# Kernel tuning notes

Hardware: AMD Instinct MI355X
Metric: run time of the kernel (lower is better)

Reference implementation:

```python
import jax, jax.numpy as jnp
import numpy as np

NUM_EMBEDDINGS = 1024
EMBEDDING_DIM = 64
COMMITMENT_COST = 0.25


def setup_inputs() -> dict:
    key = jax.random.key(0)
    k1, k2 = jax.random.split(key)
    inputs = jax.random.normal(k1, (16, 64, 64, 64), dtype=jnp.float32)
    codebook = jax.random.normal(k2, (EMBEDDING_DIM, NUM_EMBEDDINGS), dtype=jnp.float32) * 0.01
    return {"inputs": inputs, "codebook": codebook}


def reference(inputs, codebook):
    # flatten exactly as torch: reshape(-1, D) on (B,C,H,W)
    flat = inputs.reshape(-1, EMBEDDING_DIM)  # [N, D]
    distances = (jnp.sum(flat * flat, axis=1, keepdims=True)
                 + jnp.sum(codebook * codebook, axis=0, keepdims=True)
                 - 2.0 * jnp.matmul(flat, codebook))
    encoding_indices = jnp.argmin(distances, axis=1)  # [N]
    quantized = codebook[:, encoding_indices].T.reshape(inputs.shape)
    # losses (MSE over all elements)
    codebook_loss = jnp.mean((jax.lax.stop_gradient(quantized) - inputs) ** 2)
    commitment_loss = COMMITMENT_COST * jnp.mean((quantized - jax.lax.stop_gradient(inputs)) ** 2)
    # perplexity from codebook usage histogram
    n = encoding_indices.shape[0]
    counts = jnp.zeros((NUM_EMBEDDINGS,), dtype=jnp.float32).at[encoding_indices].add(1.0)
    avg_probs = counts / n
    entropy = -jnp.sum(avg_probs * jnp.log(avg_probs + 1e-10))
    perplexity = jnp.exp(entropy)
    # straight-through estimator
    ste = inputs + jax.lax.stop_gradient(quantized - inputs)
    return (ste, perplexity, codebook_loss, commitment_loss,
            encoding_indices.reshape(inputs.shape[0], -1))
```

## Files before the change

kernel.cpp:

```cpp
#include <hip/hip_runtime.h>

typedef __attribute__((ext_vector_type(8))) short short8;
typedef __attribute__((ext_vector_type(4))) float f32x4;

#define N_ROWS   65536
#define DIM      64
#define K_CODES  1024
#define TOTAL_ELEMS 4194304
#define THETA    1e-3f


__device__ __forceinline__ unsigned short f2bf(float f) {
    union { float f; unsigned int u; } c; c.f = f;
    unsigned int u = c.u;
    return (unsigned short)((u + 0x7fffu + ((u >> 16) & 1u)) >> 16);
}
__device__ __forceinline__ float bf2f(unsigned short b) {
    union { unsigned int u; float f; } c; c.u = ((unsigned int)b) << 16;
    return c.f;
}
__device__ __forceinline__ f32x4 MFMA(short8 a, short8 b, f32x4 c) {
    return __builtin_amdgcn_mfma_f32_16x16x32_bf16(a, b, c, 0, 0, 0);
}

__global__ __launch_bounds__(128) void k_prep(const float* __restrict__ cb,
                                              float* __restrict__ norms,
                                              int* __restrict__ counts,
                                              float* __restrict__ cbT,
                                              unsigned short* __restrict__ cb_hi,
                                              unsigned short* __restrict__ cb_lo,
                                              int* __restrict__ flagcnt) {
    int k = blockIdx.x * 128 + threadIdx.x;
    float v0 = cb[k];
    float s = __fmul_rn(v0, v0);
    cbT[k * DIM] = v0;
    {
        float t = -2.0f * v0;
        unsigned short hb = f2bf(t);
        cb_hi[k * DIM] = hb;
        cb_lo[k * DIM] = f2bf(t - bf2f(hb));
    }
#pragma unroll 4
    for (int d = 1; d < DIM; ++d) {
        float v = cb[d * K_CODES + k];
        s = __fadd_rn(s, __fmul_rn(v, v));
        cbT[k * DIM + d] = v;
        float t = -2.0f * v;
        unsigned short hb = f2bf(t);
        cb_hi[k * DIM + d] = hb;
        cb_lo[k * DIM + d] = f2bf(t - bf2f(hb));
    }
    norms[k] = s;
    counts[k] = 0;
    if (k == 0) flagcnt[0] = 0;
}

__global__ __launch_bounds__(256, 2) void k_assign(const float* __restrict__ x,
                                                   const float* __restrict__ norms,
                                                   const unsigned short* __restrict__ cb_hi,
                                                   const unsigned short* __restrict__ cb_lo,
                                                   int* __restrict__ idx_out,
                                                   int* __restrict__ flagcnt,
                                                   int* __restrict__ flaglist) {
    __shared__ __align__(16) unsigned short xs_hi[64 * 64];
    __shared__ __align__(16) unsigned short xs_lo[64 * 64];
    __shared__ float xxs[64];
    __shared__ float mv1[4][64];
    __shared__ float mv2[4][64];
    __shared__ int   mk1[4][64];

    const int tid = threadIdx.x;
    const int r0 = blockIdx.x * 64;
    const int wave = tid >> 6, lane = tid & 63;
    const int lr = lane & 15, lg = lane >> 4;

#pragma unroll
    for (int i = 0; i < 2; ++i) {
        int c = i * 256 + tid;
        int row = c >> 3, ch = c & 7;
        const float4* src = reinterpret_cast<const float4*>(x + (size_t)(r0 + row) * DIM + ch * 8);
        float4 f0 = src[0], f1 = src[1];
        float f[8] = {f0.x, f0.y, f0.z, f0.w, f1.x, f1.y, f1.z, f1.w};
        union { short8 v; unsigned short u[8]; } h, l;
#pragma unroll
        for (int j = 0; j < 8; ++j) {
            unsigned short hb = f2bf(f[j]);
            h.u[j] = hb;
            l.u[j] = f2bf(f[j] - bf2f(hb));
        }
        int eo = row * 64 + ((((ch * 16) ^ ((row & 7) << 4))) >> 1);
        *reinterpret_cast<short8*>(&xs_hi[eo]) = h.v;
        *reinterpret_cast<short8*>(&xs_lo[eo]) = l.v;
    }
    if (lane < 16) {
        int row = wave * 16 + lane;
        const float* xr = x + (size_t)(r0 + row) * DIM;
        float r[8];
#pragma unroll
        for (int j = 0; j < 8; ++j) { float v = xr[j]; r[j] = __fmul_rn(v, v); }
#pragma unroll
        for (int m = 1; m < 8; ++m)
#pragma unroll
            for (int j = 0; j < 8; ++j) { float v = xr[8 * m + j]; r[j] = __fadd_rn(r[j], __fmul_rn(v, v)); }
        float t01 = __fadd_rn(r[0], r[1]), t23 = __fadd_rn(r[2], r[3]);
        float t45 = __fadd_rn(r[4], r[5]), t67 = __fadd_rn(r[6], r[7]);
        xxs[row] = __fadd_rn(__fadd_rn(t01, t23), __fadd_rn(t45, t67));
    }
    __syncthreads();

    short8 a_hi[4][2], a_lo[4][2];
#pragma unroll
    for (int rt = 0; rt < 4; ++rt)
#pragma unroll
        for (int kh = 0; kh < 2; ++kh) {
            int row = rt * 16 + lr;
            int bo = (kh * 64 + lg * 16) ^ ((row & 7) << 4);
            int eo = row * 64 + (bo >> 1);
            a_hi[rt][kh] = *reinterpret_cast<const short8*>(&xs_hi[eo]);
            a_lo[rt][kh] = *reinterpret_cast<const short8*>(&xs_lo[eo]);
        }
    float xxv[16];
#pragma unroll
    for (int rt = 0; rt < 4; ++rt)
#pragma unroll
        for (int r = 0; r < 4; ++r) xxv[rt * 4 + r] = xxs[rt * 16 + lg * 4 + r];

    float v1[16], v2[16]; int k1[16];
#pragma unroll
    for (int i = 0; i < 16; ++i) { v1[i] = 3.4e38f; v2[i] = 3.4e38f; k1[i] = 0; }

    const short8* ph = reinterpret_cast<const short8*>(cb_hi) + (size_t)(wave * 256 + lr) * 8;
    const short8* pl = reinterpret_cast<const short8*>(cb_lo) + (size_t)(wave * 256 + lr) * 8;
    const float*  pe = norms + wave * 256 + lr;

    short8 nh0 = ph[lg], nh1 = ph[4 + lg];
    short8 nl0 = pl[lg], nl1 = pl[4 + lg];
    float  nee = *pe;

    for (int ct = 0; ct < 16; ++ct) {
        short8 h0 = nh0, h1 = nh1, l0 = nl0, l1 = nl1;
        float ee = nee;
        if (ct < 15) {
            ph += 128; pl += 128; pe += 16;
            nh0 = ph[lg]; nh1 = ph[4 + lg];
            nl0 = pl[lg]; nl1 = pl[4 + lg];
            nee = *pe;
        }
        int code = wave * 256 + ct * 16 + lr;

#pragma unroll
        for (int rt = 0; rt < 4; ++rt) {
            f32x4 acc;
            acc[0] = __fadd_rn(xxv[rt * 4 + 0], ee);
            acc[1] = __fadd_rn(xxv[rt * 4 + 1], ee);
            acc[2] = __fadd_rn(xxv[rt * 4 + 2], ee);
            acc[3] = __fadd_rn(xxv[rt * 4 + 3], ee);
            acc = MFMA(a_hi[rt][0], h0, acc);
            acc = MFMA(a_hi[rt][1], h1, acc);
            acc = MFMA(a_hi[rt][0], l0, acc);
            acc = MFMA(a_hi[rt][1], l1, acc);
            acc = MFMA(a_lo[rt][0], h0, acc);
            acc = MFMA(a_lo[rt][1], h1, acc);
#pragma unroll
            for (int r = 0; r < 4; ++r) {
                int i = rt * 4 + r;
                float d = acc[r];
                bool lt = d < v1[i];
                v2[i] = lt ? v1[i] : fminf(v2[i], d);
                k1[i] = lt ? code : k1[i];
                v1[i] = lt ? d : v1[i];
            }
        }
    }

#pragma unroll
    for (int i = 0; i < 16; ++i) {
        float a1 = v1[i], a2 = v2[i]; int ak = k1[i];
#pragma unroll
        for (int off = 1; off <= 8; off <<= 1) {
            float o1 = __shfl_xor(a1, off);
            float o2 = __shfl_xor(a2, off);
            int   ok = __shfl_xor(ak, off);
            float n2 = fminf(fmaxf(a1, o1), fminf(a2, o2));
            if (o1 < a1 || (o1 == a1 && ok < ak)) { a1 = o1; ak = ok; }
            a2 = n2;
        }
        if (lr == 0) {
            int row = (i >> 2) * 16 + lg * 4 + (i & 3);
            mv1[wave][row] = a1; mv2[wave][row] = a2; mk1[wave][row] = ak;
        }
    }
    __syncthreads();

    if (tid < 64) {
        float V1 = mv1[0][tid], V2 = mv2[0][tid]; int K1 = mk1[0][tid];
#pragma unroll
        for (int w = 1; w < 4; ++w) {
            float a1 = mv1[w][tid], a2 = mv2[w][tid]; int ak = mk1[w][tid];
            float n2 = fminf(fmaxf(V1, a1), fminf(V2, a2));
            if (a1 < V1) { V1 = a1; K1 = ak; }
            V2 = n2;
        }
        int rg = r0 + tid;
        idx_out[rg] = K1;
        if (V2 - V1 <= THETA) {
            int p = atomicAdd(flagcnt, 1);
            flaglist[p] = rg;
        }
    }
}

__global__ __launch_bounds__(256) void k_exact(const float* __restrict__ x,
                                               const float* __restrict__ cb,
                                               const float* __restrict__ norms,
                                               const int* __restrict__ flagcnt,
                                               const int* __restrict__ flaglist,
                                               int* __restrict__ idx) {
    __shared__ __align__(16) float xrow[8][64];
    __shared__ float xxs[8];
    __shared__ int rlist[8];
    __shared__ float lv[8][4];
    __shared__ int   lk[8][4];

    const int tid = threadIdx.x;
    const int lane = tid & 63, wv = tid >> 6;
    const int cnt = flagcnt[0];
    const int ngroups = (cnt + 7) >> 3;

    for (int g = blockIdx.x; g < ngroups; g += gridDim.x) {
        const int base = g * 8;
        const int rem = min(8, cnt - base);
        __syncthreads();
        if (tid < 8)
            rlist[tid] = flaglist[base + ((tid < rem) ? tid : 0)];
        __syncthreads();
#pragma unroll
        for (int i = 0; i < 2; ++i) {
            int e = i * 256 + tid;
            int r = e >> 6, d = e & 63;
            xrow[r][d] = x[(size_t)rlist[r] * DIM + d];
        }
        __syncthreads();
        if (tid < 8) {
            float rr[8];
#pragma unroll
            for (int j = 0; j < 8; ++j) { float v = xrow[tid][j]; rr[j] = __fmul_rn(v, v); }
#pragma unroll
            for (int m = 1; m < 8; ++m)
#pragma unroll
                for (int j = 0; j < 8; ++j) { float v = xrow[tid][8 * m + j]; rr[j] = __fadd_rn(rr[j], __fmul_rn(v, v)); }
            float t01 = __fadd_rn(rr[0], rr[1]), t23 = __fadd_rn(rr[2], rr[3]);
            float t45 = __fadd_rn(rr[4], rr[5]), t67 = __fadd_rn(rr[6], rr[7]);
            xxs[tid] = __fadd_rn(__fadd_rn(t01, t23), __fadd_rn(t45, t67));
        }
        __syncthreads();

        double acc[8][4];
#pragma unroll
        for (int r = 0; r < 8; ++r)
#pragma unroll
            for (int j = 0; j < 4; ++j) acc[r][j] = 0.0;

        for (int dc = 0; dc < DIM; dc += 4) {
            float4 xv[8];
#pragma unroll
            for (int r = 0; r < 8; ++r)
                xv[r] = *reinterpret_cast<const float4*>(&xrow[r][dc]);
            float c[4][4];
#pragma unroll
            for (int dd = 0; dd < 4; ++dd)
#pragma unroll
                for (int j = 0; j < 4; ++j)
                    c[j][dd] = cb[(size_t)(dc + dd) * K_CODES + j * 256 + tid];
#pragma unroll
            for (int j = 0; j < 4; ++j)
#pragma unroll
                for (int r = 0; r < 8; ++r) {
                    acc[r][j] += (double)xv[r].x * (double)c[j][0];
                    acc[r][j] += (double)xv[r].y * (double)c[j][1];
                    acc[r][j] += (double)xv[r].z * (double)c[j][2];
                    acc[r][j] += (double)xv[r].w * (double)c[j][3];
                }
        }

#pragma unroll
        for (int r = 0; r < 8; ++r) {
            float xx = xxs[r];
            float bv = 3.4e38f; int bk = 0x7fffffff;
#pragma unroll
            for (int j = 0; j < 4; ++j) {
                int k = j * 256 + tid;
                float m = (float)acc[r][j];
                float dist = __fsub_rn(__fadd_rn(xx, norms[k]), __fmul_rn(2.0f, m));
                if (dist < bv) { bv = dist; bk = k; }
            }
#pragma unroll
            for (int off = 1; off <= 32; off <<= 1) {
                float ov = __shfl_xor(bv, off); int ok = __shfl_xor(bk, off);
                if (ov < bv || (ov == bv && ok < bk)) { bv = ov; bk = ok; }
            }
            if (lane == 0) { lv[r][wv] = bv; lk[r][wv] = bk; }
        }
        __syncthreads();
        if (tid < rem) {
            float bv = lv[tid][0]; int bk = lk[tid][0];
#pragma unroll
            for (int w = 1; w < 4; ++w)
                if (lv[tid][w] < bv || (lv[tid][w] == bv && lk[tid][w] < bk)) { bv = lv[tid][w]; bk = lk[tid][w]; }
            idx[rlist[tid]] = bk;
        }
    }
}

__global__ __launch_bounds__(256) void k_quant(const float* __restrict__ x,
                                               const float* __restrict__ cbT,
                                               const int* __restrict__ idx,
                                               float* __restrict__ ste,
                                               float* __restrict__ partials,
                                               int* __restrict__ counts,
                                               float* __restrict__ idxf) {
    int t  = blockIdx.x * 256 + threadIdx.x;
    int e  = t << 2;
    int n  = e >> 6;
    int dc = e & 63;
    float4 xv = *reinterpret_cast<const float4*>(x + e);
    int k = idx[n];
    float4 qv = *reinterpret_cast<const float4*>(cbT + (size_t)k * DIM + dc);

    float4 sv;
    sv.x = xv.x + (qv.x - xv.x);
    sv.y = xv.y + (qv.y - xv.y);
    sv.z = xv.z + (qv.z - xv.z);
    sv.w = xv.w + (qv.w - xv.w);
    *reinterpret_cast<float4*>(ste + e) = sv;

    if (dc == 0) {
        atomicAdd(&counts[k], 1);
        idxf[n] = (float)k;
    }

    float dx = qv.x - xv.x, dy = qv.y - xv.y, dz = qv.z - xv.z, dw = qv.w - xv.w;
    float s = dx * dx + dy * dy + dz * dz + dw * dw;

#pragma unroll
    for (int off = 32; off >= 1; off >>= 1) s += __shfl_down(s, off);
    __shared__ float red[4];
    int wave = threadIdx.x >> 6, lane = threadIdx.x & 63;
    if (lane == 0) red[wave] = s;
    __syncthreads();
    if (threadIdx.x == 0)
        partials[blockIdx.x] = (red[0] + red[1]) + (red[2] + red[3]);
}

__global__ __launch_bounds__(1024) void k_final(const float* __restrict__ partials,
                                                const int* __restrict__ counts,
                                                float* __restrict__ out_scalars) {
    int tid = threadIdx.x;
    float s = 0.f;
    for (int i = tid; i < 4096; i += 1024) s += partials[i];
#pragma unroll
    for (int off = 32; off >= 1; off >>= 1) s += __shfl_down(s, off);
    __shared__ float wsum[16];
    int wave = tid >> 6, lane = tid & 63;
    if (lane == 0) wsum[wave] = s;

    float c = (float)counts[tid];
    float p = c * (1.0f / 65536.0f);
    float t = -p * logf(p + 1e-10f);
#pragma unroll
    for (int off = 32; off >= 1; off >>= 1) t += __shfl_down(t, off);
    __shared__ float esum[16];
    if (lane == 0) esum[wave] = t;
    __syncthreads();

    if (tid == 0) {
        float total = 0.f, ent = 0.f;
        for (int w = 0; w < 16; ++w) { total += wsum[w]; ent += esum[w]; }
        float mean = total * (1.0f / (float)TOTAL_ELEMS);
        out_scalars[0] = expf(ent);
        out_scalars[1] = mean;
        out_scalars[2] = 0.25f * mean;
    }
}

extern "C" void kernel_launch(void* const* d_in, const int* in_sizes, int n_in,
                              void* d_out, int out_size, void* d_ws, size_t ws_size,
                              hipStream_t stream) {
    const float* x  = (const float*)d_in[0];
    const float* cb = (const float*)d_in[1];
    float* out = (float*)d_out;
    float* ws  = (float*)d_ws;

    float* norms    = ws;
    int*   idx      = (int*)(ws + 1024);
    int*   counts   = (int*)(ws + 66560);
    float* partials = ws + 67584;
    float* cbT      = ws + 71680;
    unsigned short* cb_hi = (unsigned short*)(ws + 137216);
    unsigned short* cb_lo = (unsigned short*)(ws + 169984);
    int*   flagcnt  = (int*)(ws + 202752);
    int*   flaglist = (int*)(ws + 202753);

    float* ste     = out;
    float* scalars = out + TOTAL_ELEMS;
    float* idxf    = out + TOTAL_ELEMS + 3;

    k_prep  <<<8,    128, 0, stream>>>(cb, norms, counts, cbT, cb_hi, cb_lo, flagcnt);
    k_assign<<<1024, 256, 0, stream>>>(x, norms, cb_hi, cb_lo, idx, flagcnt, flaglist);
    k_exact <<<1024, 256, 0, stream>>>(x, cb, norms, flagcnt, flaglist, idx);
    k_quant <<<4096, 256, 0, stream>>>(x, cbT, idx, ste, partials, counts, idxf);
    k_final <<<1,   1024, 0, stream>>>(partials, counts, scalars);
}
```

Measured before the change: 124.7 us.

## Halve rows per assign block, raise occupancy, drop row-norm term from distances

The assign kernel now handles 32 rows per block instead of 64, launches twice as many blocks, and asks for 4 blocks per CU instead of 2. Each thread's A fragments and running-min state shrink by half, lowering register pressure. The per-row ||x||^2 term is removed from the accumulator init, since it is constant per row and does not change the argmin or the top-two gap. The cost is that every block still streams the full hi/lo codebook, so total codebook traffic from cache doubles while MFMA work per load halves.

```diff
diff --git a/kernel.cpp b/kernel.cpp
--- a/kernel.cpp
+++ b/kernel.cpp
@@ -8,6 +8,7 @@
 #define K_CODES  1024
 #define TOTAL_ELEMS 4194304
 #define THETA    1e-3f
+#define ROWS_PB  32
 
 
 __device__ __forceinline__ unsigned short f2bf(float f) {
@@ -55,29 +56,26 @@
     if (k == 0) flagcnt[0] = 0;
 }
 
-__global__ __launch_bounds__(256, 2) void k_assign(const float* __restrict__ x,
+__global__ __launch_bounds__(256, 4) void k_assign(const float* __restrict__ x,
                                                    const float* __restrict__ norms,
                                                    const unsigned short* __restrict__ cb_hi,
                                                    const unsigned short* __restrict__ cb_lo,
                                                    int* __restrict__ idx_out,
                                                    int* __restrict__ flagcnt,
                                                    int* __restrict__ flaglist) {
-    __shared__ __align__(16) unsigned short xs_hi[64 * 64];
-    __shared__ __align__(16) unsigned short xs_lo[64 * 64];
-    __shared__ float xxs[64];
-    __shared__ float mv1[4][64];
-    __shared__ float mv2[4][64];
-    __shared__ int   mk1[4][64];
+    __shared__ __align__(16) unsigned short xs_hi[ROWS_PB * 64];
+    __shared__ __align__(16) unsigned short xs_lo[ROWS_PB * 64];
+    __shared__ float mv1[4][ROWS_PB];
+    __shared__ float mv2[4][ROWS_PB];
+    __shared__ int   mk1[4][ROWS_PB];
 
     const int tid = threadIdx.x;
-    const int r0 = blockIdx.x * 64;
+    const int r0 = blockIdx.x * ROWS_PB;
     const int wave = tid >> 6, lane = tid & 63;
     const int lr = lane & 15, lg = lane >> 4;
 
-#pragma unroll
-    for (int i = 0; i < 2; ++i) {
-        int c = i * 256 + tid;
-        int row = c >> 3, ch = c & 7;
+    {
+        int row = tid >> 3, ch = tid & 7;
         const float4* src = reinterpret_cast<const float4*>(x + (size_t)(r0 + row) * DIM + ch * 8);
         float4 f0 = src[0], f1 = src[1];
         float f[8] = {f0.x, f0.y, f0.z, f0.w, f1.x, f1.y, f1.z, f1.w};
@@ -92,25 +90,11 @@
         *reinterpret_cast<short8*>(&xs_hi[eo]) = h.v;
         *reinterpret_cast<short8*>(&xs_lo[eo]) = l.v;
     }
-    if (lane < 16) {
-        int row = wave * 16 + lane;
-        const float* xr = x + (size_t)(r0 + row) * DIM;
-        float r[8];
-#pragma unroll
-        for (int j = 0; j < 8; ++j) { float v = xr[j]; r[j] = __fmul_rn(v, v); }
-#pragma unroll
-        for (int m = 1; m < 8; ++m)
-#pragma unroll
-            for (int j = 0; j < 8; ++j) { float v = xr[8 * m + j]; r[j] = __fadd_rn(r[j], __fmul_rn(v, v)); }
-        float t01 = __fadd_rn(r[0], r[1]), t23 = __fadd_rn(r[2], r[3]);
-        float t45 = __fadd_rn(r[4], r[5]), t67 = __fadd_rn(r[6], r[7]);
-        xxs[row] = __fadd_rn(__fadd_rn(t01, t23), __fadd_rn(t45, t67));
-    }
     __syncthreads();
 
-    short8 a_hi[4][2], a_lo[4][2];
-#pragma unroll
-    for (int rt = 0; rt < 4; ++rt)
+    short8 a_hi[2][2], a_lo[2][2];
+#pragma unroll
+    for (int rt = 0; rt < 2; ++rt)
 #pragma unroll
         for (int kh = 0; kh < 2; ++kh) {
             int row = rt * 16 + lr;
@@ -119,15 +103,10 @@
             a_hi[rt][kh] = *reinterpret_cast<const short8*>(&xs_hi[eo]);
             a_lo[rt][kh] = *reinterpret_cast<const short8*>(&xs_lo[eo]);
         }
-    float xxv[16];
-#pragma unroll
-    for (int rt = 0; rt < 4; ++rt)
-#pragma unroll
-        for (int r = 0; r < 4; ++r) xxv[rt * 4 + r] = xxs[rt * 16 + lg * 4 + r];
-
-    float v1[16], v2[16]; int k1[16];
-#pragma unroll
-    for (int i = 0; i < 16; ++i) { v1[i] = 3.4e38f; v2[i] = 3.4e38f; k1[i] = 0; }
+
+    float v1[8], v2[8]; int k1[8];
+#pragma unroll
+    for (int i = 0; i < 8; ++i) { v1[i] = 3.4e38f; v2[i] = 3.4e38f; k1[i] = 0; }
 
     const short8* ph = reinterpret_cast<const short8*>(cb_hi) + (size_t)(wave * 256 + lr) * 8;
     const short8* pl = reinterpret_cast<const short8*>(cb_lo) + (size_t)(wave * 256 + lr) * 8;
@@ -149,12 +128,8 @@
         int code = wave * 256 + ct * 16 + lr;
 
 #pragma unroll
-        for (int rt = 0; rt < 4; ++rt) {
-            f32x4 acc;
-            acc[0] = __fadd_rn(xxv[rt * 4 + 0], ee);
-            acc[1] = __fadd_rn(xxv[rt * 4 + 1], ee);
-            acc[2] = __fadd_rn(xxv[rt * 4 + 2], ee);
-            acc[3] = __fadd_rn(xxv[rt * 4 + 3], ee);
+        for (int rt = 0; rt < 2; ++rt) {
+            f32x4 acc = {ee, ee, ee, ee};
             acc = MFMA(a_hi[rt][0], h0, acc);
             acc = MFMA(a_hi[rt][1], h1, acc);
             acc = MFMA(a_hi[rt][0], l0, acc);
@@ -174,7 +149,7 @@
     }
 
 #pragma unroll
-    for (int i = 0; i < 16; ++i) {
+    for (int i = 0; i < 8; ++i) {
         float a1 = v1[i], a2 = v2[i]; int ak = k1[i];
 #pragma unroll
         for (int off = 1; off <= 8; off <<= 1) {
@@ -192,7 +167,7 @@
     }
     __syncthreads();
 
-    if (tid < 64) {
+    if (tid < ROWS_PB) {
         float V1 = mv1[0][tid], V2 = mv2[0][tid]; int K1 = mk1[0][tid];
 #pragma unroll
         for (int w = 1; w < 4; ++w) {
@@ -406,7 +381,7 @@
     float* idxf    = out + TOTAL_ELEMS + 3;
 
     k_prep  <<<8,    128, 0, stream>>>(cb, norms, counts, cbT, cb_hi, cb_lo, flagcnt);
-    k_assign<<<1024, 256, 0, stream>>>(x, norms, cb_hi, cb_lo, idx, flagcnt, flaglist);
+    k_assign<<<2048, 256, 0, stream>>>(x, norms, cb_hi, cb_lo, idx, flagcnt, flaglist);
     k_exact <<<1024, 256, 0, stream>>>(x, cb, norms, flagcnt, flaglist, idx);
     k_quant <<<4096, 256, 0, stream>>>(x, cbT, idx, ste, partials, counts, idxf);
     k_final <<<1,   1024, 0, stream>>>(partials, counts, scalars);
```

After: 169.3 us. +35.8%, slower.
